# Kernel tuning notes

Hardware: AMD Instinct MI355X
Metric: run time of the kernel (lower is better)

The kernel has to match this reference:

```python
import jax, jax.numpy as jnp
import numpy as np

B, C, N = 8, 512, 2048  # batch, channels (=size), tokens


def setup_inputs() -> dict:
    key = jax.random.key(0)
    ks = jax.random.split(key, 9)
    s = 1.0 / np.sqrt(C)
    return {
        "q": jax.random.normal(ks[0], (B, C, N), dtype=jnp.float32),
        "k": jax.random.normal(ks[1], (B, C, N), dtype=jnp.float32),
        "v": jax.random.normal(ks[2], (B, C, N), dtype=jnp.float32),
        "wq": jax.random.normal(ks[3], (C, C), dtype=jnp.float32) * s,
        "bq": jax.random.normal(ks[4], (C,), dtype=jnp.float32) * s,
        "wk": jax.random.normal(ks[5], (C, C), dtype=jnp.float32) * s,
        "bk": jax.random.normal(ks[6], (C,), dtype=jnp.float32) * s,
        "wv": jax.random.normal(ks[7], (C, C), dtype=jnp.float32) * s,
        "bv": jax.random.normal(ks[8], (C,), dtype=jnp.float32) * s,
    }


def _proj(x, w, b):
    # 1x1 conv over channels: out[b,c,n] = sum_i w[c,i] x[b,i,n] + b[c]
    return jnp.einsum('ci,bin->bcn', w, x) + b[None, :, None]


def reference(q, k, v, wq, bq, wk, bk, wv, bv):
    residual = q                                   # [B, C, N]
    qp = _proj(q, wq, bq).transpose(0, 2, 1)       # [B, N, C]
    kp = _proj(k, wk, bk).transpose(0, 2, 1)       # [B, N, C]
    vp = _proj(v, wv, bv).transpose(0, 2, 1)       # [B, N, C]
    attn = jnp.einsum('bnc,bmc->bnm', qp, kp)      # raw QK^T, no scale/softmax
    out = jnp.einsum('bnm,bmc->bnc', attn, vp)     # [B, N, C]
    return out.transpose(0, 2, 1) + residual       # [B, C, N]
```

## Files before the change

### kernel.cpp

```cpp
#include <hip/hip_runtime.h>
#include <hip/hip_bf16.h>
#include <stdint.h>

#define B_ 8
#define C_ 512
#define N_ 2048

typedef __bf16 bf16_t;
typedef bf16_t bf16x8 __attribute__((ext_vector_type(8)));
typedef bf16_t bf16x4 __attribute__((ext_vector_type(4)));
typedef float f32x4 __attribute__((ext_vector_type(4)));

__global__ __launch_bounds__(256) void prep_qw_kernel(
    const float* __restrict__ q,
    const float* __restrict__ wq, const float* __restrict__ wk,
    const float* __restrict__ wv, const float* __restrict__ bq,
    const float* __restrict__ bk,
    bf16_t* __restrict__ qT,
    bf16_t* __restrict__ WqT, bf16_t* __restrict__ WkT, bf16_t* __restrict__ Wvb,
    float* __restrict__ s1p)
{
    __shared__ bf16_t tile[64][65];
    __shared__ float red256[256];
    const int bid = blockIdx.x;
    const int tid = threadIdx.x;

    if (bid < 2048) {
        const int b = bid >> 8;
        const int rem = bid & 255;
        const int c0 = (rem >> 5) * 64;
        const int n0 = (rem & 31) * 64;
        const float* src = q + (size_t)b * C_ * N_;
        bf16_t* dT = qT + (size_t)b * N_ * C_;
        const int cx = (tid & 15) * 4, ry = tid >> 4;
#pragma unroll
        for (int r = ry; r < 64; r += 16) {
            float4 f = *(const float4*)&src[(size_t)(c0 + r) * N_ + n0 + cx];
            tile[r][cx + 0] = (bf16_t)f.x; tile[r][cx + 1] = (bf16_t)f.y;
            tile[r][cx + 2] = (bf16_t)f.z; tile[r][cx + 3] = (bf16_t)f.w;
        }
        __syncthreads();
#pragma unroll
        for (int r = ry; r < 64; r += 16) {
            bf16x4 o;
            o[0] = tile[cx + 0][r]; o[1] = tile[cx + 1][r];
            o[2] = tile[cx + 2][r]; o[3] = tile[cx + 3][r];
            *(bf16x4*)&dT[(size_t)(n0 + r) * C_ + c0 + cx] = o;
        }
    } else if (bid < 2176) {
        const int t = bid - 2048;
        const float* src = (t < 64) ? wq : wk;
        bf16_t* dst = (t < 64) ? WqT : WkT;
        const int j = t & 63;
        const int i0 = (j & 7) * 64, c0 = (j >> 3) * 64;
        const int cx = (tid & 15) * 4, ry = tid >> 4;
#pragma unroll
        for (int r = ry; r < 64; r += 16) {
            float4 f = *(const float4*)&src[(size_t)(c0 + r) * C_ + i0 + cx];
            tile[r][cx + 0] = (bf16_t)f.x; tile[r][cx + 1] = (bf16_t)f.y;
            tile[r][cx + 2] = (bf16_t)f.z; tile[r][cx + 3] = (bf16_t)f.w;
        }
        __syncthreads();
#pragma unroll
        for (int r = ry; r < 64; r += 16) {
            bf16x4 o;
            o[0] = tile[cx + 0][r]; o[1] = tile[cx + 1][r];
            o[2] = tile[cx + 2][r]; o[3] = tile[cx + 3][r];
            *(bf16x4*)&dst[(size_t)(i0 + r) * C_ + c0 + cx] = o;
        }
    } else if (bid < 2240) {
        const int j = bid - 2176;
#pragma unroll
        for (int p = 0; p < 4; ++p) {
            const int i = j * 4096 + p * 1024 + tid * 4;
            float4 f = *(const float4*)(wv + i);
            bf16x4 o;
            o[0] = (bf16_t)f.x; o[1] = (bf16_t)f.y;
            o[2] = (bf16_t)f.z; o[3] = (bf16_t)f.w;
            *(bf16x4*)(Wvb + i) = o;
        }
    } else {
        float p = bk[tid] * bq[tid] + bk[tid + 256] * bq[tid + 256];
        red256[tid] = p;
        __syncthreads();
        for (int s = 128; s > 0; s >>= 1) {
            if (tid < s) red256[tid] += red256[tid + s];
            __syncthreads();
        }
        if (tid == 0) s1p[0] = red256[0];
    }
}

__global__ __launch_bounds__(256) void dkv_M_kernel(
    const float* __restrict__ Kin, const float* __restrict__ Vin,
    bf16_t* __restrict__ Dp, float* __restrict__ sk4, float* __restrict__ sv4,
    const bf16_t* __restrict__ WqT, const bf16_t* __restrict__ WkT,
    bf16_t* __restrict__ M, const float* __restrict__ bq,
    const float* __restrict__ bk, float* __restrict__ gk,
    float* __restrict__ va)
{
    __shared__ __align__(16) float AsF[128 * 64];
    __shared__ __align__(16) float BsF[128 * 64];

    const int f = blockIdx.x;
    const int tid = threadIdx.x, lane = tid & 63, wave = tid >> 6;
    const int wr = wave >> 1, wc = wave & 1;
    const size_t sCC = (size_t)C_ * C_;

    if (f < 512) {
        const int xcd = f & 7, sl = f >> 3;
        const int g = xcd + 8 * (sl >> 4), t5 = sl & 15;
        const int bz = g >> 2, sp = g & 3;
        const int m0 = (t5 >> 2) * 128, n0 = (t5 & 3) * 128;
        const int kbeg = sp * 512;

        const float* Ab = Kin + (size_t)bz * C_ * N_;
        const float* Bb = Vin + (size_t)bz * C_ * N_;

        f32x4 acc[4][4];
#pragma unroll
        for (int i = 0; i < 4; ++i)
#pragma unroll
            for (int j = 0; j < 4; ++j) acc[i][j] = 0.f;

        const int prow = tid >> 4;
        const int cs   = (tid & 15) ^ (prow & 7);
        const int ldso = tid * 16;

        const int srr = tid >> 1, hh = tid & 1;
        float hsA = 0.f, hsB = 0.f;
        const bool doA = (n0 == 0), doB = (m0 == 0);

        for (int t = 0; t < 8; ++t) {
            const float* ga = Ab + (size_t)(m0 + prow) * N_ + kbeg + t * 64 + cs * 4;
            const float* gb = Bb + (size_t)(n0 + prow) * N_ + kbeg + t * 64 + cs * 4;
#pragma unroll
            for (int p = 0; p < 8; ++p)
                __builtin_amdgcn_global_load_lds(
                    (const __attribute__((address_space(1))) void*)(ga + (size_t)p * 16 * N_),
                    (__attribute__((address_space(3))) void*)((char*)AsF + ldso + p * 4096),
                    16, 0, 0);
#pragma unroll
            for (int p = 0; p < 8; ++p)
                __builtin_amdgcn_global_load_lds(
                    (const __attribute__((address_space(1))) void*)(gb + (size_t)p * 16 * N_),
                    (__attribute__((address_space(3))) void*)((char*)BsF + ldso + p * 4096),
                    16, 0, 0);
            __syncthreads();

#pragma unroll
            for (int kk = 0; kk < 64; kk += 32) {
                bf16x8 af[4], bfr[4];
                const int kcol = kk + (lane >> 4) * 8;
                const int c1 = kcol >> 2;
#pragma unroll
                for (int m = 0; m < 4; ++m) {
                    const int r = wr * 64 + (lane & 15) + m * 16;
                    f32x4 lo = *(const f32x4*)((const char*)AsF + r * 256 + ((c1 ^ (r & 7)) << 4));
                    f32x4 hi = *(const f32x4*)((const char*)AsF + r * 256 + (((c1 + 1) ^ (r & 7)) << 4));
                    bf16x8 fr;
                    fr[0] = (bf16_t)lo[0]; fr[1] = (bf16_t)lo[1];
                    fr[2] = (bf16_t)lo[2]; fr[3] = (bf16_t)lo[3];
                    fr[4] = (bf16_t)hi[0]; fr[5] = (bf16_t)hi[1];
                    fr[6] = (bf16_t)hi[2]; fr[7] = (bf16_t)hi[3];
                    af[m] = fr;
                }
#pragma unroll
                for (int n = 0; n < 4; ++n) {
                    const int r = wc * 64 + (lane & 15) + n * 16;
                    f32x4 lo = *(const f32x4*)((const char*)BsF + r * 256 + ((c1 ^ (r & 7)) << 4));
                    f32x4 hi = *(const f32x4*)((const char*)BsF + r * 256 + (((c1 + 1) ^ (r & 7)) << 4));
                    bf16x8 fr;
                    fr[0] = (bf16_t)lo[0]; fr[1] = (bf16_t)lo[1];
                    fr[2] = (bf16_t)lo[2]; fr[3] = (bf16_t)lo[3];
                    fr[4] = (bf16_t)hi[0]; fr[5] = (bf16_t)hi[1];
                    fr[6] = (bf16_t)hi[2]; fr[7] = (bf16_t)hi[3];
                    bfr[n] = fr;
                }
#pragma unroll
                for (int m = 0; m < 4; ++m)
#pragma unroll
                    for (int n = 0; n < 4; ++n)
                        acc[m][n] = __builtin_amdgcn_mfma_f32_16x16x32_bf16(
                            af[m], bfr[n], acc[m][n], 0, 0, 0);
            }

            if (doA) {
#pragma unroll
                for (int u = 0; u < 8; ++u) {
                    const int slot = ((hh * 8 + u) + srr) & 15;
                    f32x4 vv = *(const f32x4*)((const char*)AsF + srr * 256 + slot * 16);
                    hsA += vv[0] + vv[1] + vv[2] + vv[3];
                }
            }
            if (doB) {
#pragma unroll
                for (int u = 0; u < 8; ++u) {
                    const int slot = ((hh * 8 + u) + srr) & 15;
                    f32x4 vv = *(const f32x4*)((const char*)BsF + srr * 256 + slot * 16);
                    hsB += vv[0] + vv[1] + vv[2] + vv[3];
                }
            }
            __syncthreads();
        }

        const int rj = (lane >> 4) * 4;
        const int cc = lane & 15;
        const int z = bz * 4 + sp;
#pragma unroll
        for (int m = 0; m < 4; ++m)
#pragma unroll
            for (int n = 0; n < 4; ++n) {
                const int col = n0 + wc * 64 + n * 16 + cc;
                f32x4 vv = acc[m][n];
#pragma unroll
                for (int j = 0; j < 4; ++j) {
                    const int row = m0 + wr * 64 + m * 16 + rj + j;
                    Dp[(size_t)z * sCC + (size_t)row * C_ + col] = (bf16_t)vv[j];
                }
            }
        if (doA) {
            hsA += __shfl_xor(hsA, 1, 64);
            if (!hh) sk4[(size_t)(sp * B_ + bz) * C_ + m0 + srr] = hsA;
        }
        if (doB) {
            hsB += __shfl_xor(hsB, 1, 64);
            if (!hh) sv4[(size_t)(sp * B_ + bz) * C_ + n0 + srr] = hsB;
        }
    } else if (f < 576) {
        bf16_t* As = (bf16_t*)AsF;
        bf16_t* Bs = (bf16_t*)BsF;
        const int g = f - 512;
        const int m0 = (g >> 3) * 64, n0 = (g & 7) * 64;
        f32x4 acc[2][2];
#pragma unroll
        for (int i = 0; i < 2; ++i)
#pragma unroll
            for (int j = 0; j < 2; ++j) acc[i][j] = 0.f;
        const int srow = tid >> 3;
        const int scol = ((tid & 7) ^ (srow & 7)) * 8;
        const int ldso = tid * 16;
        for (int t = 0; t < 8; ++t) {
            const bf16_t* ga = WqT + (size_t)(m0 + srow) * C_ + t * 64 + scol;
            const bf16_t* gb = WkT + (size_t)(n0 + srow) * C_ + t * 64 + scol;
#pragma unroll
            for (int p = 0; p < 2; ++p)
                __builtin_amdgcn_global_load_lds(
                    (const __attribute__((address_space(1))) void*)(ga + (size_t)p * 32 * C_),
                    (__attribute__((address_space(3))) void*)((char*)As + ldso + p * 4096),
                    16, 0, 0);
#pragma unroll
            for (int p = 0; p < 2; ++p)
                __builtin_amdgcn_global_load_lds(
                    (const __attribute__((address_space(1))) void*)(gb + (size_t)p * 32 * C_),
                    (__attribute__((address_space(3))) void*)((char*)Bs + ldso + p * 4096),
                    16, 0, 0);
            __syncthreads();
#pragma unroll
            for (int kk = 0; kk < 64; kk += 32) {
                bf16x8 af[2], bfr[2];
                const int kcol = kk + (lane >> 4) * 8;
                const int kcn = kcol >> 3;
#pragma unroll
                for (int m = 0; m < 2; ++m) {
                    const int r = wr * 32 + (lane & 15) + m * 16;
                    af[m] = *(const bf16x8*)((const char*)As + r * 128 +
                                             ((kcn ^ (r & 7)) << 4));
                }
#pragma unroll
                for (int n = 0; n < 2; ++n) {
                    const int r = wc * 32 + (lane & 15) + n * 16;
                    bfr[n] = *(const bf16x8*)((const char*)Bs + r * 128 +
                                              ((kcn ^ (r & 7)) << 4));
                }
#pragma unroll
                for (int m = 0; m < 2; ++m)
#pragma unroll
                    for (int n = 0; n < 2; ++n)
                        acc[m][n] = __builtin_amdgcn_mfma_f32_16x16x32_bf16(
                            af[m], bfr[n], acc[m][n], 0, 0, 0);
            }
            __syncthreads();
        }
        const int rj = (lane >> 4) * 4;
        const int cc = lane & 15;
#pragma unroll
        for (int m = 0; m < 2; ++m)
#pragma unroll
            for (int n = 0; n < 2; ++n) {
                const int col = n0 + wc * 32 + n * 16 + cc;
                f32x4 vv = acc[m][n];
#pragma unroll
                for (int j = 0; j < 4; ++j) {
                    const int row = m0 + wr * 32 + m * 16 + rj + j;
                    M[(size_t)row * C_ + col] = (bf16_t)vv[j];
                }
            }
    } else {
        const int j = f - 576;
        const bf16_t* W = (j < 8) ? WkT : WqT;
        const float* bb = (j < 8) ? bq : bk;
        float* out = (j < 8) ? gk : va;
        const int row = (j & 7) * 64 + (tid >> 2);
        const int c0 = (tid & 3) * 128;
        const bf16_t* rp = W + (size_t)row * C_ + c0;
        float acc = 0.f;
#pragma unroll
        for (int e = 0; e < 128; e += 8) {
            bf16x8 vv = *(const bf16x8*)(rp + e);
#pragma unroll
            for (int x = 0; x < 8; ++x) acc += (float)vv[x] * bb[c0 + e + x];
        }
        acc += __shfl_xor(acc, 1, 64);
        acc += __shfl_xor(acc, 2, 64);
        if ((tid & 3) == 0) out[row] = acc;
    }
}

__global__ __launch_bounds__(256) void p1_fused_kernel(
    const bf16_t* __restrict__ Wvb, const bf16_t* __restrict__ Dp,
    bf16_t* __restrict__ P1, const bf16_t* __restrict__ M,
    const float* __restrict__ sk4, const float* __restrict__ sv4,
    const float* __restrict__ gk, const float* __restrict__ s1p,
    float* __restrict__ u, float* __restrict__ vbraw, float* __restrict__ s2)
{
    __shared__ __align__(16) bf16_t As[64 * 64];
    __shared__ __align__(16) bf16_t Bs[64 * 64];
    __shared__ float svec[C_];
    __shared__ float red[256];
    const int f = blockIdx.x;
    const int tid = threadIdx.x, lane = tid & 63, wave = tid >> 6;
    const int wr = wave >> 1, wc = wave & 1;
    const size_t sCC = (size_t)C_ * C_;
    const size_t st = (size_t)B_ * C_;

    if (f < 512) {
        const int bz = f >> 6;
        const int m0 = ((f >> 3) & 7) * 64, n0 = (f & 7) * 64;
        f32x4 acc[2][2];
#pragma unroll
        for (int i = 0; i < 2; ++i)
#pragma unroll
            for (int j = 0; j < 2; ++j) acc[i][j] = 0.f;
        const int srow = tid >> 3;
        const int scol = ((tid & 7) ^ (srow & 7)) * 8;
        const int ldso = tid * 16;

        for (int sp = 0; sp < 4; ++sp) {
            const bf16_t* Bb = Dp + (size_t)(bz * 4 + sp) * sCC;
            for (int t = 0; t < 8; ++t) {
                const bf16_t* ga = Wvb + (size_t)(m0 + srow) * C_ + t * 64 + scol;
                const bf16_t* gb = Bb + (size_t)(n0 + srow) * C_ + t * 64 + scol;
#pragma unroll
                for (int p = 0; p < 2; ++p)
                    __builtin_amdgcn_global_load_lds(
                        (const __attribute__((address_space(1))) void*)(ga + (size_t)p * 32 * C_),
                        (__attribute__((address_space(3))) void*)((char*)As + ldso + p * 4096),
                        16, 0, 0);
#pragma unroll
                for (int p = 0; p < 2; ++p)
                    __builtin_amdgcn_global_load_lds(
                        (const __attribute__((address_space(1))) void*)(gb + (size_t)p * 32 * C_),
                        (__attribute__((address_space(3))) void*)((char*)Bs + ldso + p * 4096),
                        16, 0, 0);
                __syncthreads();
#pragma unroll
                for (int kk = 0; kk < 64; kk += 32) {
                    bf16x8 af[2], bfr[2];
                    const int kcol = kk + (lane >> 4) * 8;
                    const int kcn = kcol >> 3;
#pragma unroll
                    for (int m = 0; m < 2; ++m) {
                        const int r = wr * 32 + (lane & 15) + m * 16;
                        af[m] = *(const bf16x8*)((const char*)As + r * 128 +
                                                 ((kcn ^ (r & 7)) << 4));
                    }
#pragma unroll
                    for (int n = 0; n < 2; ++n) {
                        const int r = wc * 32 + (lane & 15) + n * 16;
                        bfr[n] = *(const bf16x8*)((const char*)Bs + r * 128 +
                                                  ((kcn ^ (r & 7)) << 4));
                    }
#pragma unroll
                    for (int m = 0; m < 2; ++m)
#pragma unroll
                        for (int n = 0; n < 2; ++n)
                            acc[m][n] = __builtin_amdgcn_mfma_f32_16x16x32_bf16(
                                af[m], bfr[n], acc[m][n], 0, 0, 0);
                }
                __syncthreads();
            }
        }
        const int rj = (lane >> 4) * 4;
        const int cc = lane & 15;
#pragma unroll
        for (int m = 0; m < 2; ++m)
#pragma unroll
            for (int n = 0; n < 2; ++n) {
                const int col = n0 + wc * 32 + n * 16 + cc;
                f32x4 vv = acc[m][n];
#pragma unroll
                for (int j = 0; j < 4; ++j) {
                    const int row = m0 + wr * 32 + m * 16 + rj + j;
                    P1[(size_t)bz * sCC + (size_t)row * C_ + col] = (bf16_t)vv[j];
                }
            }
    } else if (f < 520) {
        const int b = f - 512;
        const float* s4 = sv4 + (size_t)b * C_;
#pragma unroll
        for (int rr = 0; rr < 2; ++rr) {
            const int j = tid * 2 + rr;
            svec[j] = s4[j] + s4[st + j] + s4[2 * st + j] + s4[3 * st + j];
        }
        __syncthreads();
        const int c = tid * 2;
#pragma unroll
        for (int rr = 0; rr < 2; ++rr) {
            const bf16_t* row = Wvb + (size_t)(c + rr) * C_;
            float acc = 0.f;
            for (int j = 0; j < C_; j += 8) {
                bf16x8 vv = *(const bf16x8*)(row + j);
#pragma unroll
                for (int e = 0; e < 8; ++e) acc += (float)vv[e] * svec[j + e];
            }
            u[b * C_ + c + rr] = acc;
        }
    } else {
        const int b = f - 520;
        const float* s4 = sk4 + (size_t)b * C_;
#pragma unroll
        for (int rr = 0; rr < 2; ++rr) {
            const int j = tid * 2 + rr;
            svec[j] = s4[j] + s4[st + j] + s4[2 * st + j] + s4[3 * st + j];
        }
        __syncthreads();
        const int c = tid * 2;
#pragma unroll
        for (int rr = 0; rr < 2; ++rr) {
            const bf16_t* row = M + (size_t)(c + rr) * C_;
            float acc = 0.f;
            for (int j = 0; j < C_; j += 8) {
                bf16x8 vv = *(const bf16x8*)(row + j);
#pragma unroll
                for (int e = 0; e < 8; ++e) acc += (float)vv[e] * svec[j + e];
            }
            vbraw[b * C_ + c + rr] = acc;
        }
        float p = svec[tid] * gk[tid] + svec[tid + 256] * gk[tid + 256];
        red[tid] = p;
        __syncthreads();
        for (int s = 128; s > 0; s >>= 1) {
            if (tid < s) red[tid] += red[tid + s];
            __syncthreads();
        }
        if (tid == 0) s2[b] = red[0] + 2048.0f * s1p[0];
    }
}

__global__ __launch_bounds__(256) void gemm_ht(
    const bf16_t* __restrict__ A, const bf16_t* __restrict__ Bm,
    bf16_t* __restrict__ Cout,
    const float* __restrict__ e0, const float* __restrict__ e1,
    const float* __restrict__ e2, const float* __restrict__ e3,
    const float* __restrict__ bqv, float* __restrict__ hout,
    const float* __restrict__ s1p, const float* __restrict__ s2p)
{
    __shared__ __align__(16) bf16_t As[64 * 64];
    __shared__ __align__(16) bf16_t Bs[64 * 64];

    const int tid = threadIdx.x, lane = tid & 63, wave = tid >> 6;
    const int wr = wave >> 1, wc = wave & 1;
    const int bz = blockIdx.z;
    const int m0 = blockIdx.y * 64, n0 = blockIdx.x * 64;
    const size_t sCC = (size_t)C_ * C_;

    const bf16_t* Ab = A + (size_t)bz * sCC;

    f32x4 acc[2][2];
#pragma unroll
    for (int i = 0; i < 2; ++i)
#pragma unroll
        for (int j = 0; j < 2; ++j) acc[i][j] = 0.f;

    const int srow = tid >> 3;
    const int scol = ((tid & 7) ^ (srow & 7)) * 8;
    const int ldso = tid * 16;

    float hacc = 0.f;
    const bool doH = (blockIdx.x == 0);

    for (int t = 0; t < 8; ++t) {
        const bf16_t* ga = Ab + (size_t)(m0 + srow) * C_ + t * 64 + scol;
        const bf16_t* gb = Bm + (size_t)(n0 + srow) * C_ + t * 64 + scol;
#pragma unroll
        for (int p = 0; p < 2; ++p)
            __builtin_amdgcn_global_load_lds(
                (const __attribute__((address_space(1))) void*)(ga + (size_t)p * 32 * C_),
                (__attribute__((address_space(3))) void*)((char*)As + ldso + p * 4096),
                16, 0, 0);
#pragma unroll
        for (int p = 0; p < 2; ++p)
            __builtin_amdgcn_global_load_lds(
                (const __attribute__((address_space(1))) void*)(gb + (size_t)p * 32 * C_),
                (__attribute__((address_space(3))) void*)((char*)Bs + ldso + p * 4096),
                16, 0, 0);
        __syncthreads();

#pragma unroll
        for (int kk = 0; kk < 64; kk += 32) {
            bf16x8 af[2], bfr[2];
            const int kcol = kk + (lane >> 4) * 8;
            const int kcn = kcol >> 3;
#pragma unroll
            for (int m = 0; m < 2; ++m) {
                const int r = wr * 32 + (lane & 15) + m * 16;
                af[m] = *(const bf16x8*)((const char*)As + r * 128 +
                                         ((kcn ^ (r & 7)) << 4));
            }
#pragma unroll
            for (int n = 0; n < 2; ++n) {
                const int r = wc * 32 + (lane & 15) + n * 16;
                bfr[n] = *(const bf16x8*)((const char*)Bs + r * 128 +
                                          ((kcn ^ (r & 7)) << 4));
            }
#pragma unroll
            for (int m = 0; m < 2; ++m)
#pragma unroll
                for (int n = 0; n < 2; ++n)
                    acc[m][n] = __builtin_amdgcn_mfma_f32_16x16x32_bf16(
                        af[m], bfr[n], acc[m][n], 0, 0, 0);
        }
        if (doH) {
            const int rr = tid >> 2, qq = tid & 3;
#pragma unroll
            for (int uq = 0; uq < 2; ++uq) {
                const int c = qq * 2 + uq;
                bf16x8 av = *(const bf16x8*)((const char*)As + rr * 128 +
                                             ((c ^ (rr & 7)) << 4));
                const float* bp = bqv + t * 64 + c * 8;
#pragma unroll
                for (int e = 0; e < 8; ++e) hacc += (float)av[e] * bp[e];
            }
        }
        __syncthreads();
    }

    const int rj = (lane >> 4) * 4;
    const int cc = lane & 15;
#pragma unroll
    for (int m = 0; m < 2; ++m) {
#pragma unroll
        for (int n = 0; n < 2; ++n) {
            const int col = n0 + wc * 32 + n * 16 + cc;
            f32x4 vv = acc[m][n];
#pragma unroll
            for (int j = 0; j < 4; ++j) {
                const int row = m0 + wr * 32 + m * 16 + rj + j;
                float val = vv[j] + e0[bz * C_ + row] * e1[col] +
                            e2[row] * (e3[bz * C_ + col] + 2048.0f * e1[col]);
                Cout[(size_t)bz * sCC + (size_t)row * C_ + col] = (bf16_t)val;
            }
        }
    }
    if (doH) {
        hacc += __shfl_xor(hacc, 1, 64);
        hacc += __shfl_xor(hacc, 2, 64);
        if ((tid & 3) == 0) {
            const int row = m0 + (tid >> 2);
            hout[bz * C_ + row] = hacc + e0[bz * C_ + row] * s1p[0] +
                                  e2[row] * s2p[bz];
        }
    }
}

__global__ __launch_bounds__(256) void gemm_final(
    const bf16_t* __restrict__ A, const bf16_t* __restrict__ Bm,
    float* __restrict__ Cout, const float* __restrict__ qres,
    const float* __restrict__ hvec)
{
    __shared__ __align__(16) bf16_t As[128 * 64];
    __shared__ __align__(16) bf16_t Bs[128 * 64];

    const int f = blockIdx.x;
    const int xcd = f & 7, sl = f >> 3;
    const int g = xcd + 8 * (sl >> 2);
    const int m0 = (sl & 3) * 128;
    const int bz = g >> 4;
    const int n0 = (g & 15) * 128;
    const int K = C_;

    const int tid = threadIdx.x, lane = tid & 63, wave = tid >> 6;
    const int wr = wave >> 1, wc = wave & 1;

    const bf16_t* Ab = A + (size_t)bz * ((size_t)C_ * C_);
    const bf16_t* Bb = Bm + (size_t)bz * ((size_t)N_ * C_);

    f32x4 acc[4][4];
#pragma unroll
    for (int i = 0; i < 4; ++i)
#pragma unroll
        for (int j = 0; j < 4; ++j) acc[i][j] = 0.f;

    const int srow = tid >> 3;
    const int scol = ((tid & 7) ^ (srow & 7)) * 8;
    const int ldso = tid * 16;

    for (int t = 0; t < 8; ++t) {
        const bf16_t* ga = Ab + (size_t)(m0 + srow) * K + t * 64 + scol;
        const bf16_t* gb = Bb + (size_t)(n0 + srow) * K + t * 64 + scol;
#pragma unroll
        for (int p = 0; p < 4; ++p)
            __builtin_amdgcn_global_load_lds(
                (const __attribute__((address_space(1))) void*)(ga + (size_t)p * 32 * K),
                (__attribute__((address_space(3))) void*)((char*)As + ldso + p * 4096),
                16, 0, 0);
#pragma unroll
        for (int p = 0; p < 4; ++p)
            __builtin_amdgcn_global_load_lds(
                (const __attribute__((address_space(1))) void*)(gb + (size_t)p * 32 * K),
                (__attribute__((address_space(3))) void*)((char*)Bs + ldso + p * 4096),
                16, 0, 0);
        __syncthreads();

#pragma unroll
        for (int kk = 0; kk < 64; kk += 32) {
            bf16x8 af[4], bfr[4];
            const int kcol = kk + (lane >> 4) * 8;
            const int kcn = kcol >> 3;
#pragma unroll
            for (int m = 0; m < 4; ++m) {
                const int r = wr * 64 + (lane & 15) + m * 16;
                af[m] = *(const bf16x8*)((const char*)As + r * 128 +
                                         ((kcn ^ (r & 7)) << 4));
            }
#pragma unroll
            for (int n = 0; n < 4; ++n) {
                const int r = wc * 64 + (lane & 15) + n * 16;
                bfr[n] = *(const bf16x8*)((const char*)Bs + r * 128 +
                                          ((kcn ^ (r & 7)) << 4));
            }
#pragma unroll
            for (int m = 0; m < 4; ++m)
#pragma unroll
                for (int n = 0; n < 4; ++n)
                    acc[m][n] = __builtin_amdgcn_mfma_f32_16x16x32_bf16(
                        af[m], bfr[n], acc[m][n], 0, 0, 0);
        }
        __syncthreads();
    }

    const int rj = (lane >> 4) * 4;
    const int cc = lane & 15;
    const size_t ob = (size_t)bz * ((size_t)C_ * N_);
#pragma unroll
    for (int m = 0; m < 4; ++m) {
#pragma unroll
        for (int n = 0; n < 4; ++n) {
            const int col = n0 + wc * 64 + n * 16 + cc;
            f32x4 vv = acc[m][n];
#pragma unroll
            for (int j = 0; j < 4; ++j) {
                const int row = m0 + wr * 64 + m * 16 + rj + j;
                const size_t o = ob + (size_t)row * N_ + col;
                Cout[o] = vv[j] + hvec[bz * C_ + row] + qres[o];
            }
        }
    }
}

extern "C" void kernel_launch(void* const* d_in, const int* in_sizes, int n_in,
                              void* d_out, int out_size, void* d_ws, size_t ws_size,
                              hipStream_t stream)
{
    (void)in_sizes; (void)n_in; (void)out_size; (void)ws_size;
    const float* q  = (const float*)d_in[0];
    const float* k  = (const float*)d_in[1];
    const float* v  = (const float*)d_in[2];
    const float* wq = (const float*)d_in[3];
    const float* bq = (const float*)d_in[4];
    const float* wk = (const float*)d_in[5];
    const float* bk = (const float*)d_in[6];
    const float* wv = (const float*)d_in[7];
    const float* bv = (const float*)d_in[8];
    float* out = (float*)d_out;

    char* ws = (char*)d_ws;
    const size_t WSZ = (size_t)C_ * C_ * 2;
    const size_t TSZ = (size_t)B_ * N_ * C_ * 2;
    const size_t SCZ = (size_t)B_ * C_ * C_ * 2;
    const size_t VSZ = (size_t)B_ * C_ * 4;
    size_t off = 0;
    bf16_t* WqTb = (bf16_t*)(ws + off); off += WSZ;
    bf16_t* WkTb = (bf16_t*)(ws + off); off += WSZ;
    bf16_t* Wvb  = (bf16_t*)(ws + off); off += WSZ;
    bf16_t* M    = (bf16_t*)(ws + off); off += WSZ;
    bf16_t* qT   = (bf16_t*)(ws + off); off += TSZ;
    bf16_t* Dp   = (bf16_t*)(ws + off); off += TSZ;
    bf16_t* P1   = (bf16_t*)(ws + off); off += SCZ;
    bf16_t* HT   = (bf16_t*)(ws + off); off += SCZ;
    float*  sk4  = (float*)(ws + off);  off += 4 * VSZ;
    float*  sv4  = (float*)(ws + off);  off += 4 * VSZ;
    float*  gk   = (float*)(ws + off);  off += C_ * 4;
    float*  va   = (float*)(ws + off);  off += C_ * 4;
    float*  s1p  = (float*)(ws + off);  off += 64;
    float*  s2   = (float*)(ws + off);  off += 64;
    float*  uu   = (float*)(ws + off);  off += VSZ;
    float*  vbr  = (float*)(ws + off);  off += VSZ;
    float*  hb   = (float*)(ws + off);  off += VSZ;

    const dim3 blk(256);

    prep_qw_kernel<<<dim3(2241), blk, 0, stream>>>(
        q, wq, wk, wv, bq, bk, qT, WqTb, WkTb, Wvb, s1p);

    dkv_M_kernel<<<dim3(592), blk, 0, stream>>>(
        k, v, Dp, sk4, sv4, WqTb, WkTb, M, bq, bk, gk, va);

    p1_fused_kernel<<<dim3(528), blk, 0, stream>>>(
        Wvb, Dp, P1, M, sk4, sv4, gk, s1p, uu, vbr, s2);

    gemm_ht<<<dim3(8, 8, B_), blk, 0, stream>>>(
        P1, M, HT, uu, va, bv, vbr, gk, hb, s1p, s2);

    gemm_final<<<dim3(512), blk, 0, stream>>>(HT, qT, out, q, hb);
}
```

Measured before the change: 102.7 us.

## Move M and gk/va weight-only blocks from dkv kernel into p1 kernel

The weight-only work (the M=WqT·WkT GEMM blocks and the gk/va vector blocks) moves out of the K·V^T kernel and into the following p1 kernel, so the dkv launch now holds only the 512 heavy Dp blocks. Because M is now written in the same launch that needs it, the vbraw path is recomputed as WqT·(Wk·s) using the fp32 wk and a staged intermediate, and the s2 scalar uses bq·tv in place of gk. The intent is to balance per-launch work and drop the tail of extra blocks in the heavy kernel, at the cost of an extra matrix-vector pass and 80 more blocks in p1.

```diff
diff --git a/kernel.cpp b/kernel.cpp
--- a/kernel.cpp
+++ b/kernel.cpp
@@ -91,13 +91,9 @@
     }
 }
 
-__global__ __launch_bounds__(256) void dkv_M_kernel(
+__global__ __launch_bounds__(256) void dkv_kernel(
     const float* __restrict__ Kin, const float* __restrict__ Vin,
-    bf16_t* __restrict__ Dp, float* __restrict__ sk4, float* __restrict__ sv4,
-    const bf16_t* __restrict__ WqT, const bf16_t* __restrict__ WkT,
-    bf16_t* __restrict__ M, const float* __restrict__ bq,
-    const float* __restrict__ bk, float* __restrict__ gk,
-    float* __restrict__ va)
+    bf16_t* __restrict__ Dp, float* __restrict__ sk4, float* __restrict__ sv4)
 {
     __shared__ __align__(16) float AsF[128 * 64];
     __shared__ __align__(16) float BsF[128 * 64];
@@ -107,129 +103,221 @@
     const int wr = wave >> 1, wc = wave & 1;
     const size_t sCC = (size_t)C_ * C_;
 
+    const int xcd = f & 7, sl = f >> 3;
+    const int g = xcd + 8 * (sl >> 4), t5 = sl & 15;
+    const int bz = g >> 2, sp = g & 3;
+    const int m0 = (t5 >> 2) * 128, n0 = (t5 & 3) * 128;
+    const int kbeg = sp * 512;
+
+    const float* Ab = Kin + (size_t)bz * C_ * N_;
+    const float* Bb = Vin + (size_t)bz * C_ * N_;
+
+    f32x4 acc[4][4];
+#pragma unroll
+    for (int i = 0; i < 4; ++i)
+#pragma unroll
+        for (int j = 0; j < 4; ++j) acc[i][j] = 0.f;
+
+    const int prow = tid >> 4;
+    const int cs   = (tid & 15) ^ (prow & 7);
+    const int ldso = tid * 16;
+
+    const int srr = tid >> 1, hh = tid & 1;
+    float hsA = 0.f, hsB = 0.f;
+    const bool doA = (n0 == 0), doB = (m0 == 0);
+
+    for (int t = 0; t < 8; ++t) {
+        const float* ga = Ab + (size_t)(m0 + prow) * N_ + kbeg + t * 64 + cs * 4;
+        const float* gb = Bb + (size_t)(n0 + prow) * N_ + kbeg + t * 64 + cs * 4;
+#pragma unroll
+        for (int p = 0; p < 8; ++p)
+            __builtin_amdgcn_global_load_lds(
+                (const __attribute__((address_space(1))) void*)(ga + (size_t)p * 16 * N_),
+                (__attribute__((address_space(3))) void*)((char*)AsF + ldso + p * 4096),
+                16, 0, 0);
+#pragma unroll
+        for (int p = 0; p < 8; ++p)
+            __builtin_amdgcn_global_load_lds(
+                (const __attribute__((address_space(1))) void*)(gb + (size_t)p * 16 * N_),
+                (__attribute__((address_space(3))) void*)((char*)BsF + ldso + p * 4096),
+                16, 0, 0);
+        __syncthreads();
+
+#pragma unroll
+        for (int kk = 0; kk < 64; kk += 32) {
+            bf16x8 af[4], bfr[4];
+            const int kcol = kk + (lane >> 4) * 8;
+            const int c1 = kcol >> 2;
+#pragma unroll
+            for (int m = 0; m < 4; ++m) {
+                const int r = wr * 64 + (lane & 15) + m * 16;
+                f32x4 lo = *(const f32x4*)((const char*)AsF + r * 256 + ((c1 ^ (r & 7)) << 4));
+                f32x4 hi = *(const f32x4*)((const char*)AsF + r * 256 + (((c1 + 1) ^ (r & 7)) << 4));
+                bf16x8 fr;
+                fr[0] = (bf16_t)lo[0]; fr[1] = (bf16_t)lo[1];
+                fr[2] = (bf16_t)lo[2]; fr[3] = (bf16_t)lo[3];
+                fr[4] = (bf16_t)hi[0]; fr[5] = (bf16_t)hi[1];
+                fr[6] = (bf16_t)hi[2]; fr[7] = (bf16_t)hi[3];
+                af[m] = fr;
+            }
+#pragma unroll
+            for (int n = 0; n < 4; ++n) {
+                const int r = wc * 64 + (lane & 15) + n * 16;
+                f32x4 lo = *(const f32x4*)((const char*)BsF + r * 256 + ((c1 ^ (r & 7)) << 4));
+                f32x4 hi = *(const f32x4*)((const char*)BsF + r * 256 + (((c1 + 1) ^ (r & 7)) << 4));
+                bf16x8 fr;
+                fr[0] = (bf16_t)lo[0]; fr[1] = (bf16_t)lo[1];
+                fr[2] = (bf16_t)lo[2]; fr[3] = (bf16_t)lo[3];
+                fr[4] = (bf16_t)hi[0]; fr[5] = (bf16_t)hi[1];
+                fr[6] = (bf16_t)hi[2]; fr[7] = (bf16_t)hi[3];
+                bfr[n] = fr;
+            }
+#pragma unroll
+            for (int m = 0; m < 4; ++m)
+#pragma unroll
+                for (int n = 0; n < 4; ++n)
+                    acc[m][n] = __builtin_amdgcn_mfma_f32_16x16x32_bf16(
+                        af[m], bfr[n], acc[m][n], 0, 0, 0);
+        }
+
+        if (doA) {
+#pragma unroll
+            for (int u = 0; u < 8; ++u) {
+                const int slot = ((hh * 8 + u) + srr) & 15;
+                f32x4 vv = *(const f32x4*)((const char*)AsF + srr * 256 + slot * 16);
+                hsA += vv[0] + vv[1] + vv[2] + vv[3];
+            }
+        }
+        if (doB) {
+#pragma unroll
+            for (int u = 0; u < 8; ++u) {
+                const int slot = ((hh * 8 + u) + srr) & 15;
+                f32x4 vv = *(const f32x4*)((const char*)BsF + srr * 256 + slot * 16);
+                hsB += vv[0] + vv[1] + vv[2] + vv[3];
+            }
+        }
+        __syncthreads();
+    }
+
+    const int rj = (lane >> 4) * 4;
+    const int cc = lane & 15;
+    const int z = bz * 4 + sp;
+#pragma unroll
+    for (int m = 0; m < 4; ++m)
+#pragma unroll
+        for (int n = 0; n < 4; ++n) {
+            const int col = n0 + wc * 64 + n * 16 + cc;
+            f32x4 vv = acc[m][n];
+#pragma unroll
+            for (int j = 0; j < 4; ++j) {
+                const int row = m0 + wr * 64 + m * 16 + rj + j;
+                Dp[(size_t)z * sCC + (size_t)row * C_ + col] = (bf16_t)vv[j];
+            }
+        }
+    if (doA) {
+        hsA += __shfl_xor(hsA, 1, 64);
+        if (!hh) sk4[(size_t)(sp * B_ + bz) * C_ + m0 + srr] = hsA;
+    }
+    if (doB) {
+        hsB += __shfl_xor(hsB, 1, 64);
+        if (!hh) sv4[(size_t)(sp * B_ + bz) * C_ + n0 + srr] = hsB;
+    }
+}
+
+__global__ __launch_bounds__(256) void p1_fused_kernel(
+    const bf16_t* __restrict__ Wvb, const bf16_t* __restrict__ Dp,
+    bf16_t* __restrict__ P1,
+    const bf16_t* __restrict__ WqT, const bf16_t* __restrict__ WkT,
+    bf16_t* __restrict__ M, const float* __restrict__ wkf,
+    const float* __restrict__ bq, const float* __restrict__ bk,
+    const float* __restrict__ sk4, const float* __restrict__ sv4,
+    const float* __restrict__ s1p,
+    float* __restrict__ gk, float* __restrict__ va,
+    float* __restrict__ u, float* __restrict__ vbraw, float* __restrict__ s2)
+{
+    __shared__ __align__(16) bf16_t As[64 * 64];
+    __shared__ __align__(16) bf16_t Bs[64 * 64];
+    __shared__ float svec[C_];
+    __shared__ float tv[C_];
+    __shared__ float red[256];
+    const int f = blockIdx.x;
+    const int tid = threadIdx.x, lane = tid & 63, wave = tid >> 6;
+    const int wr = wave >> 1, wc = wave & 1;
+    const size_t sCC = (size_t)C_ * C_;
+    const size_t st = (size_t)B_ * C_;
+
     if (f < 512) {
-        const int xcd = f & 7, sl = f >> 3;
-        const int g = xcd + 8 * (sl >> 4), t5 = sl & 15;
-        const int bz = g >> 2, sp = g & 3;
-        const int m0 = (t5 >> 2) * 128, n0 = (t5 & 3) * 128;
-        const int kbeg = sp * 512;
-
-        const float* Ab = Kin + (size_t)bz * C_ * N_;
-        const float* Bb = Vin + (size_t)bz * C_ * N_;
-
-        f32x4 acc[4][4];
-#pragma unroll
-        for (int i = 0; i < 4; ++i)
-#pragma unroll
-            for (int j = 0; j < 4; ++j) acc[i][j] = 0.f;
-
-        const int prow = tid >> 4;
-        const int cs   = (tid & 15) ^ (prow & 7);
+        const int bz = f >> 6;
+        const int m0 = ((f >> 3) & 7) * 64, n0 = (f & 7) * 64;
+        f32x4 acc[2][2];
+#pragma unroll
+        for (int i = 0; i < 2; ++i)
+#pragma unroll
+            for (int j = 0; j < 2; ++j) acc[i][j] = 0.f;
+        const int srow = tid >> 3;
+        const int scol = ((tid & 7) ^ (srow & 7)) * 8;
         const int ldso = tid * 16;
 
-        const int srr = tid >> 1, hh = tid & 1;
-        float hsA = 0.f, hsB = 0.f;
-        const bool doA = (n0 == 0), doB = (m0 == 0);
-
-        for (int t = 0; t < 8; ++t) {
-            const float* ga = Ab + (size_t)(m0 + prow) * N_ + kbeg + t * 64 + cs * 4;
-            const float* gb = Bb + (size_t)(n0 + prow) * N_ + kbeg + t * 64 + cs * 4;
-#pragma unroll
-            for (int p = 0; p < 8; ++p)
-                __builtin_amdgcn_global_load_lds(
-                    (const __attribute__((address_space(1))) void*)(ga + (size_t)p * 16 * N_),
-                    (__attribute__((address_space(3))) void*)((char*)AsF + ldso + p * 4096),
-                    16, 0, 0);
-#pragma unroll
-            for (int p = 0; p < 8; ++p)
-                __builtin_amdgcn_global_load_lds(
-                    (const __attribute__((address_space(1))) void*)(gb + (size_t)p * 16 * N_),
-                    (__attribute__((address_space(3))) void*)((char*)BsF + ldso + p * 4096),
-                    16, 0, 0);
-            __syncthreads();
-
-#pragma unroll
-            for (int kk = 0; kk < 64; kk += 32) {
-                bf16x8 af[4], bfr[4];
-                const int kcol = kk + (lane >> 4) * 8;
-                const int c1 = kcol >> 2;
-#pragma unroll
-                for (int m = 0; m < 4; ++m) {
-                    const int r = wr * 64 + (lane & 15) + m * 16;
-                    f32x4 lo = *(const f32x4*)((const char*)AsF + r * 256 + ((c1 ^ (r & 7)) << 4));
-                    f32x4 hi = *(const f32x4*)((const char*)AsF + r * 256 + (((c1 + 1) ^ (r & 7)) << 4));
-                    bf16x8 fr;
-                    fr[0] = (bf16_t)lo[0]; fr[1] = (bf16_t)lo[1];
-                    fr[2] = (bf16_t)lo[2]; fr[3] = (bf16_t)lo[3];
-                    fr[4] = (bf16_t)hi[0]; fr[5] = (bf16_t)hi[1];
-                    fr[6] = (bf16_t)hi[2]; fr[7] = (bf16_t)hi[3];
-                    af[m] = fr;
+        for (int sp = 0; sp < 4; ++sp) {
+            const bf16_t* Bb = Dp + (size_t)(bz * 4 + sp) * sCC;
+            for (int t = 0; t < 8; ++t) {
+                const bf16_t* ga = Wvb + (size_t)(m0 + srow) * C_ + t * 64 + scol;
+                const bf16_t* gb = Bb + (size_t)(n0 + srow) * C_ + t * 64 + scol;
+#pragma unroll
+                for (int p = 0; p < 2; ++p)
+                    __builtin_amdgcn_global_load_lds(
+                        (const __attribute__((address_space(1))) void*)(ga + (size_t)p * 32 * C_),
+                        (__attribute__((address_space(3))) void*)((char*)As + ldso + p * 4096),
+                        16, 0, 0);
+#pragma unroll
+                for (int p = 0; p < 2; ++p)
+                    __builtin_amdgcn_global_load_lds(
+                        (const __attribute__((address_space(1))) void*)(gb + (size_t)p * 32 * C_),
+                        (__attribute__((address_space(3))) void*)((char*)Bs + ldso + p * 4096),
+                        16, 0, 0);
+                __syncthreads();
+#pragma unroll
+                for (int kk = 0; kk < 64; kk += 32) {
+                    bf16x8 af[2], bfr[2];
+                    const int kcol = kk + (lane >> 4) * 8;
+                    const int kcn = kcol >> 3;
+#pragma unroll
+                    for (int m = 0; m < 2; ++m) {
+                        const int r = wr * 32 + (lane & 15) + m * 16;
+                        af[m] = *(const bf16x8*)((const char*)As + r * 128 +
+                                                 ((kcn ^ (r & 7)) << 4));
+                    }
+#pragma unroll
+                    for (int n = 0; n < 2; ++n) {
+                        const int r = wc * 32 + (lane & 15) + n * 16;
+                        bfr[n] = *(const bf16x8*)((const char*)Bs + r * 128 +
+                                                  ((kcn ^ (r & 7)) << 4));
+                    }
+#pragma unroll
+                    for (int m = 0; m < 2; ++m)
+#pragma unroll
+                        for (int n = 0; n < 2; ++n)
+                            acc[m][n] = __builtin_amdgcn_mfma_f32_16x16x32_bf16(
+                                af[m], bfr[n], acc[m][n], 0, 0, 0);
                 }
-#pragma unroll
-                for (int n = 0; n < 4; ++n) {
-                    const int r = wc * 64 + (lane & 15) + n * 16;
-                    f32x4 lo = *(const f32x4*)((const char*)BsF + r * 256 + ((c1 ^ (r & 7)) << 4));
-                    f32x4 hi = *(const f32x4*)((const char*)BsF + r * 256 + (((c1 + 1) ^ (r & 7)) << 4));
-                    bf16x8 fr;
-                    fr[0] = (bf16_t)lo[0]; fr[1] = (bf16_t)lo[1];
-                    fr[2] = (bf16_t)lo[2]; fr[3] = (bf16_t)lo[3];
-                    fr[4] = (bf16_t)hi[0]; fr[5] = (bf16_t)hi[1];
-                    fr[6] = (bf16_t)hi[2]; fr[7] = (bf16_t)hi[3];
-                    bfr[n] = fr;
-                }
-#pragma unroll
-                for (int m = 0; m < 4; ++m)
-#pragma unroll
-                    for (int n = 0; n < 4; ++n)
-                        acc[m][n] = __builtin_amdgcn_mfma_f32_16x16x32_bf16(
-                            af[m], bfr[n], acc[m][n], 0, 0, 0);
-            }
-
-            if (doA) {
-#pragma unroll
-                for (int u = 0; u < 8; ++u) {
-                    const int slot = ((hh * 8 + u) + srr) & 15;
-                    f32x4 vv = *(const f32x4*)((const char*)AsF + srr * 256 + slot * 16);
-                    hsA += vv[0] + vv[1] + vv[2] + vv[3];
-                }
-            }
-            if (doB) {
-#pragma unroll
-                for (int u = 0; u < 8; ++u) {
-                    const int slot = ((hh * 8 + u) + srr) & 15;
-                    f32x4 vv = *(const f32x4*)((const char*)BsF + srr * 256 + slot * 16);
-                    hsB += vv[0] + vv[1] + vv[2] + vv[3];
-                }
-            }
-            __syncthreads();
-        }
-
+                __syncthreads();
+            }
+        }
         const int rj = (lane >> 4) * 4;
         const int cc = lane & 15;
-        const int z = bz * 4 + sp;
-#pragma unroll
-        for (int m = 0; m < 4; ++m)
-#pragma unroll
-            for (int n = 0; n < 4; ++n) {
-                const int col = n0 + wc * 64 + n * 16 + cc;
+#pragma unroll
+        for (int m = 0; m < 2; ++m)
+#pragma unroll
+            for (int n = 0; n < 2; ++n) {
+                const int col = n0 + wc * 32 + n * 16 + cc;
                 f32x4 vv = acc[m][n];
 #pragma unroll
                 for (int j = 0; j < 4; ++j) {
-                    const int row = m0 + wr * 64 + m * 16 + rj + j;
-                    Dp[(size_t)z * sCC + (size_t)row * C_ + col] = (bf16_t)vv[j];
+                    const int row = m0 + wr * 32 + m * 16 + rj + j;
+                    P1[(size_t)bz * sCC + (size_t)row * C_ + col] = (bf16_t)vv[j];
                 }
             }
-        if (doA) {
-            hsA += __shfl_xor(hsA, 1, 64);
-            if (!hh) sk4[(size_t)(sp * B_ + bz) * C_ + m0 + srr] = hsA;
-        }
-        if (doB) {
-            hsB += __shfl_xor(hsB, 1, 64);
-            if (!hh) sv4[(size_t)(sp * B_ + bz) * C_ + n0 + srr] = hsB;
-        }
     } else if (f < 576) {
-        bf16_t* As = (bf16_t*)AsF;
-        bf16_t* Bs = (bf16_t*)BsF;
         const int g = f - 512;
         const int m0 = (g >> 3) * 64, n0 = (g & 7) * 64;
         f32x4 acc[2][2];
@@ -296,7 +384,7 @@
                     M[(size_t)row * C_ + col] = (bf16_t)vv[j];
                 }
             }
-    } else {
+    } else if (f < 592) {
         const int j = f - 576;
         const bf16_t* W = (j < 8) ? WkT : WqT;
         const float* bb = (j < 8) ? bq : bk;
@@ -314,99 +402,8 @@
         acc += __shfl_xor(acc, 1, 64);
         acc += __shfl_xor(acc, 2, 64);
         if ((tid & 3) == 0) out[row] = acc;
-    }
-}
-
-__global__ __launch_bounds__(256) void p1_fused_kernel(
-    const bf16_t* __restrict__ Wvb, const bf16_t* __restrict__ Dp,
-    bf16_t* __restrict__ P1, const bf16_t* __restrict__ M,
-    const float* __restrict__ sk4, const float* __restrict__ sv4,
-    const float* __restrict__ gk, const float* __restrict__ s1p,
-    float* __restrict__ u, float* __restrict__ vbraw, float* __restrict__ s2)
-{
-    __shared__ __align__(16) bf16_t As[64 * 64];
-    __shared__ __align__(16) bf16_t Bs[64 * 64];
-    __shared__ float svec[C_];
-    __shared__ float red[256];
-    const int f = blockIdx.x;
-    const int tid = threadIdx.x, lane = tid & 63, wave = tid >> 6;
-    const int wr = wave >> 1, wc = wave & 1;
-    const size_t sCC = (size_t)C_ * C_;
-    const size_t st = (size_t)B_ * C_;
-
-    if (f < 512) {
-        const int bz = f >> 6;
-        const int m0 = ((f >> 3) & 7) * 64, n0 = (f & 7) * 64;
-        f32x4 acc[2][2];
-#pragma unroll
-        for (int i = 0; i < 2; ++i)
-#pragma unroll
-            for (int j = 0; j < 2; ++j) acc[i][j] = 0.f;
-        const int srow = tid >> 3;
-        const int scol = ((tid & 7) ^ (srow & 7)) * 8;
-        const int ldso = tid * 16;
-
-        for (int sp = 0; sp < 4; ++sp) {
-            const bf16_t* Bb = Dp + (size_t)(bz * 4 + sp) * sCC;
-            for (int t = 0; t < 8; ++t) {
-                const bf16_t* ga = Wvb + (size_t)(m0 + srow) * C_ + t * 64 + scol;
-                const bf16_t* gb = Bb + (size_t)(n0 + srow) * C_ + t * 64 + scol;
-#pragma unroll
-                for (int p = 0; p < 2; ++p)
-                    __builtin_amdgcn_global_load_lds(
-                        (const __attribute__((address_space(1))) void*)(ga + (size_t)p * 32 * C_),
-                        (__attribute__((address_space(3))) void*)((char*)As + ldso + p * 4096),
-                        16, 0, 0);
-#pragma unroll
-                for (int p = 0; p < 2; ++p)
-                    __builtin_amdgcn_global_load_lds(
-                        (const __attribute__((address_space(1))) void*)(gb + (size_t)p * 32 * C_),
-                        (__attribute__((address_space(3))) void*)((char*)Bs + ldso + p * 4096),
-                        16, 0, 0);
-                __syncthreads();
-#pragma unroll
-                for (int kk = 0; kk < 64; kk += 32) {
-                    bf16x8 af[2], bfr[2];
-                    const int kcol = kk + (lane >> 4) * 8;
-                    const int kcn = kcol >> 3;
-#pragma unroll
-                    for (int m = 0; m < 2; ++m) {
-                        const int r = wr * 32 + (lane & 15) + m * 16;
-                        af[m] = *(const bf16x8*)((const char*)As + r * 128 +
-                                                 ((kcn ^ (r & 7)) << 4));
-                    }
-#pragma unroll
-                    for (int n = 0; n < 2; ++n) {
-                        const int r = wc * 32 + (lane & 15) + n * 16;
-                        bfr[n] = *(const bf16x8*)((const char*)Bs + r * 128 +
-                                                  ((kcn ^ (r & 7)) << 4));
-                    }
-#pragma unroll
-                    for (int m = 0; m < 2; ++m)
-#pragma unroll
-                        for (int n = 0; n < 2; ++n)
-                            acc[m][n] = __builtin_amdgcn_mfma_f32_16x16x32_bf16(
-                                af[m], bfr[n], acc[m][n], 0, 0, 0);
-                }
-                __syncthreads();
-            }
-        }
-        const int rj = (lane >> 4) * 4;
-        const int cc = lane & 15;
-#pragma unroll
-        for (int m = 0; m < 2; ++m)
-#pragma unroll
-            for (int n = 0; n < 2; ++n) {
-                const int col = n0 + wc * 32 + n * 16 + cc;
-                f32x4 vv = acc[m][n];
-#pragma unroll
-                for (int j = 0; j < 4; ++j) {
-                    const int row = m0 + wr * 32 + m * 16 + rj + j;
-                    P1[(size_t)bz * sCC + (size_t)row * C_ + col] = (bf16_t)vv[j];
-                }
-            }
-    } else if (f < 520) {
-        const int b = f - 512;
+    } else if (f < 600) {
+        const int b = f - 592;
         const float* s4 = sv4 + (size_t)b * C_;
 #pragma unroll
         for (int rr = 0; rr < 2; ++rr) {
@@ -427,7 +424,7 @@
             u[b * C_ + c + rr] = acc;
         }
     } else {
-        const int b = f - 520;
+        const int b = f - 600;
         const float* s4 = sk4 + (size_t)b * C_;
 #pragma unroll
         for (int rr = 0; rr < 2; ++rr) {
@@ -438,16 +435,28 @@
         const int c = tid * 2;
 #pragma unroll
         for (int rr = 0; rr < 2; ++rr) {
-            const bf16_t* row = M + (size_t)(c + rr) * C_;
+            const float* row = wkf + (size_t)(c + rr) * C_;
+            float acc = 0.f;
+            for (int j = 0; j < C_; j += 4) {
+                float4 ww = *(const float4*)(row + j);
+                acc += ww.x * svec[j] + ww.y * svec[j + 1] +
+                       ww.z * svec[j + 2] + ww.w * svec[j + 3];
+            }
+            tv[c + rr] = acc;
+        }
+        __syncthreads();
+#pragma unroll
+        for (int rr = 0; rr < 2; ++rr) {
+            const bf16_t* row = WqT + (size_t)(c + rr) * C_;
             float acc = 0.f;
             for (int j = 0; j < C_; j += 8) {
                 bf16x8 vv = *(const bf16x8*)(row + j);
 #pragma unroll
-                for (int e = 0; e < 8; ++e) acc += (float)vv[e] * svec[j + e];
+                for (int e = 0; e < 8; ++e) acc += (float)vv[e] * tv[j + e];
             }
             vbraw[b * C_ + c + rr] = acc;
         }
-        float p = svec[tid] * gk[tid] + svec[tid + 256] * gk[tid + 256];
+        float p = bq[tid] * tv[tid] + bq[tid + 256] * tv[tid + 256];
         red[tid] = p;
         __syncthreads();
         for (int s = 128; s > 0; s >>= 1) {
@@ -714,11 +723,11 @@
     prep_qw_kernel<<<dim3(2241), blk, 0, stream>>>(
         q, wq, wk, wv, bq, bk, qT, WqTb, WkTb, Wvb, s1p);
 
-    dkv_M_kernel<<<dim3(592), blk, 0, stream>>>(
-        k, v, Dp, sk4, sv4, WqTb, WkTb, M, bq, bk, gk, va);
-
-    p1_fused_kernel<<<dim3(528), blk, 0, stream>>>(
-        Wvb, Dp, P1, M, sk4, sv4, gk, s1p, uu, vbr, s2);
+    dkv_kernel<<<dim3(512), blk, 0, stream>>>(k, v, Dp, sk4, sv4);
+
+    p1_fused_kernel<<<dim3(608), blk, 0, stream>>>(
+        Wvb, Dp, P1, WqTb, WkTb, M, wk, bq, bk, sk4, sv4, s1p,
+        gk, va, uu, vbr, s2);
 
     gemm_ht<<<dim3(8, 8, B_), blk, 0, stream>>>(
         P1, M, HT, uu, va, bv, vbr, gk, hb, s1p, s2);
```

After: 130.3 us. 1.27x slower.
